# Optimization experiments

Hardware: AMD Instinct MI355X
Metric: run time of the kernel (lower is better)

The kernel has to match this reference:

```python
import jax, jax.numpy as jnp
import numpy as np

N_FILTER = 128
IMAGE_SIZE = 64
CHANNELS = 3
LAT_SIZE = 512
N_CALLS = 2 * 16  # n_calls * 16 sequential CA steps
EPS = 1e-5       # InstanceNorm2d default eps

_SOBEL_X = np.array([[-1.0, 0.0, 1.0], [-2.0, 0.0, 2.0], [-1.0, 0.0, 1.0]], np.float32) / 8.0
_SOBEL_Y = _SOBEL_X.T.copy()
_SOBEL_K = jnp.asarray(np.stack([_SOBEL_X, _SOBEL_Y])[:, None])  # [2,1,3,3]


def sobel_perception(x):
    # x: [B,C,H,W] -> [B,3C,H,W] = concat(identity, grad_x, grad_y)
    B, C, H, W = x.shape
    g = jax.lax.conv_general_dilated(
        x.reshape(B * C, 1, H, W), _SOBEL_K, (1, 1), 'SAME',
        dimension_numbers=('NCHW', 'OIHW', 'NCHW'))
    g = g.reshape(B, C, 2, H, W)
    return jnp.concatenate([x, g[:, :, 0], g[:, :, 1]], axis=1)


def instance_norm(x):
    # per (b, c) normalization over H, W (affine=False)
    m = jnp.mean(x, axis=(2, 3), keepdims=True)
    v = jnp.var(x, axis=(2, 3), keepdims=True)
    return (x - m) * jax.lax.rsqrt(v + EPS)


def setup_inputs() -> dict:
    key = jax.random.key(0)
    k1, k2, k3 = jax.random.split(key, 3)
    C = N_FILTER
    n_params = 3 * C * C + C  # dyn conv weight + bias
    return {
        'lat': jax.random.normal(k1, (8, LAT_SIZE), jnp.float32),
        'leak_factor': jnp.ones((), jnp.float32) * 0.1,
        'w_dyn': jax.random.normal(k2, (LAT_SIZE, n_params), jnp.float32) * 0.02,
        'b_dyn': jax.random.normal(k3, (n_params,), jnp.float32) * 0.02,
    }


def reference(lat, leak_factor, w_dyn, b_dyn):
    B = lat.shape[0]
    C, H, W = N_FILTER, IMAGE_SIZE, IMAGE_SIZE
    # ca_seed: zeros with the center cell set to 1 (Growing-NCA style seed)
    seed = jnp.zeros((B, C, H, W), lat.dtype).at[:, :, H // 2, W // 2].set(1.0)

    # latent-conditioned dynamic 1x1 conv params (per sample)
    params = lat @ w_dyn + b_dyn                     # [B, 3C*C + C]
    w = params[:, :3 * C * C].reshape(B, C, 3 * C)   # [B, out, in]
    b = params[:, 3 * C * C:]                        # [B, C]

    lf = jnp.clip(leak_factor, 0.001, 1000.0)

    def step(out, _):
        y = sobel_perception(out)                    # [B,3C,H,W]
        y = instance_norm(y)
        y = jnp.einsum('bihw,boi->bohw', y, w) + b[:, :, None, None]
        out = out + lf * y
        return out, out

    out, embs = jax.lax.scan(step, seed, None, length=N_CALLS)
    out_embs = jnp.concatenate([seed[None], embs], axis=0)  # [N_CALLS+1,B,C,H,W]
    out_raw = out[:, :CHANNELS]
    return jnp.clip(out_raw, -1.0, 1.0), out_embs, out_raw
```

## Files before the change

### kernel.cpp

```cpp
#include <hip/hip_runtime.h>

typedef unsigned short u16;
typedef short short8 __attribute__((ext_vector_type(8)));
typedef float floatx4 __attribute__((ext_vector_type(4)));

#define NB 8
#define NC 128
#define K3 384
#define HW 4096
#define LATN 512
#define NPAR 49280
#define W2OFF 49152
#define NSTEP 32

#define EMB_OFF 98304
#define EMB_SLICE 4194304
#define RAW_OFF 138510336

__device__ __forceinline__ float bf2f(u16 h) {
    return __uint_as_float(((unsigned)h) << 16);
}
__device__ __forceinline__ u16 f2bf(float f) {
    unsigned u = __float_as_uint(f);
    u += 0x7fffu + ((u >> 16) & 1u);
    return (u16)(u >> 16);
}
__device__ __forceinline__ void splitbf(float f, u16& hi, u16& lo) {
    unsigned u = __float_as_uint(f);
    hi = (u16)(u >> 16);
    lo = f2bf(f - __uint_as_float(u & 0xFFFF0000u));
}

__global__ void k_detect(const unsigned* __restrict__ lfp,
                         int* __restrict__ flag, float* __restrict__ lfF) {
    unsigned bits = lfp[0];
    int isf32 = ((bits & 0xFFFFu) == 0xCCCDu);
    float lf = isf32 ? __uint_as_float(bits) : bf2f((u16)(bits & 0xFFFFu));
    flag[0] = isf32;
    lfF[0] = fminf(fmaxf(lf, 0.001f), 1000.0f);
}

__global__ __launch_bounds__(256) void k_init(const void* __restrict__ lat,
                                              const int* __restrict__ flag,
                                              float* __restrict__ latF,
                                              float* __restrict__ state,
                                              void* __restrict__ outv) {
    int isf32 = flag[0];
    int e = blockIdx.x * 256 + threadIdx.x;
    if (e < NB * LATN)
        latF[e] = isf32 ? ((const float*)lat)[e] : bf2f(((const u16*)lat)[e]);
    float v = ((e & (HW - 1)) == 2080) ? 1.0f : 0.0f;
    state[e] = v;
    if (isf32) ((float*)outv)[EMB_OFF + e] = v;
    else       ((u16*)outv)[EMB_OFF + e] = f2bf(v);
}

__global__ __launch_bounds__(256) void k_params(const float* __restrict__ latF,
                                                const void* __restrict__ w_dyn,
                                                const void* __restrict__ b_dyn,
                                                const int* __restrict__ flag,
                                                u16* __restrict__ Wh,
                                                u16* __restrict__ Wl,
                                                float* __restrict__ biasP) {
    int isf32 = flag[0];
    int j = blockIdx.x * 256 + threadIdx.x;
    if (j >= NPAR) return;
    float acc[NB] = {};
    if (isf32) {
        const float* wd = (const float*)w_dyn;
        for (int k = 0; k < LATN; k++) {
            float wv = wd[(size_t)k * NPAR + j];
#pragma unroll
            for (int b = 0; b < NB; b++) acc[b] += latF[b * LATN + k] * wv;
        }
    } else {
        const u16* wd = (const u16*)w_dyn;
        for (int k = 0; k < LATN; k++) {
            float wv = bf2f(wd[(size_t)k * NPAR + j]);
#pragma unroll
            for (int b = 0; b < NB; b++) acc[b] += latF[b * LATN + k] * wv;
        }
    }
    float bd = isf32 ? ((const float*)b_dyn)[j] : bf2f(((const u16*)b_dyn)[j]);
    if (j < W2OFF) {
#pragma unroll
        for (int b = 0; b < NB; b++) {
            u16 hi, lo;
            splitbf(acc[b] + bd, hi, lo);
            Wh[(size_t)b * W2OFF + j] = hi;
            Wl[(size_t)b * W2OFF + j] = lo;
        }
    } else {
#pragma unroll
        for (int b = 0; b < NB; b++) biasP[b * NC + (j - W2OFF)] = acc[b] + bd;
    }
}

__global__ __launch_bounds__(256) void k_sobel(const float* __restrict__ state,
                                               u16* __restrict__ Yh,
                                               u16* __restrict__ Yl) {
    int blk = blockIdx.x;
    int b = blk >> 7, c = blk & 127;
    const float* xp = state + ((size_t)(b * NC + c)) * HW;
    __shared__ float sm[66 * 68];
    __shared__ float red[4][3];
    __shared__ float bc[6];
    int tid = threadIdx.x;
    int lane = tid & 63, w = tid >> 6;
    for (int i = tid; i < 66 * 68; i += 256) sm[i] = 0.f;
    __syncthreads();
    for (int i = tid; i < HW; i += 256)
        sm[((i >> 6) + 1) * 68 + (i & 63) + 1] = xp[i];
    __syncthreads();

    int rr = tid >> 2, c0 = (tid & 3) << 4;
    const float* r0 = sm + rr * 68 + c0;
    const float* r1 = r0 + 68;
    const float* r2 = r1 + 68;
    float xv[16], gxv[16], gyv[16];
    float a00 = r0[0], a01 = r0[1];
    float a10 = r1[0], a11 = r1[1];
    float a20 = r2[0], a21 = r2[1];
    float sx = 0, sgx = 0, sgy = 0;
#pragma unroll
    for (int u = 0; u < 16; u++) {
        float a02 = r0[u + 2], a12 = r1[u + 2], a22 = r2[u + 2];
        float x  = a11;
        float gx = (a02 - a00 + 2.f * (a12 - a10) + a22 - a20) * 0.125f;
        float gy = (a20 + 2.f * a21 + a22 - a00 - 2.f * a01 - a02) * 0.125f;
        xv[u] = x; gxv[u] = gx; gyv[u] = gy;
        sx += x; sgx += gx; sgy += gy;
        a00 = a01; a01 = a02; a10 = a11; a11 = a12; a20 = a21; a21 = a22;
    }
#pragma unroll
    for (int off = 32; off >= 1; off >>= 1) {
        sx += __shfl_down(sx, off); sgx += __shfl_down(sgx, off); sgy += __shfl_down(sgy, off);
    }
    if (lane == 0) { red[w][0] = sx; red[w][1] = sgx; red[w][2] = sgy; }
    __syncthreads();
    if (tid == 0) {
        float t0 = 0, t1 = 0, t2 = 0;
        for (int i = 0; i < 4; i++) { t0 += red[i][0]; t1 += red[i][1]; t2 += red[i][2]; }
        bc[0] = t0 * (1.f / HW); bc[1] = t1 * (1.f / HW); bc[2] = t2 * (1.f / HW);
    }
    __syncthreads();
    float mx = bc[0], mgx = bc[1], mgy = bc[2];
    float vx = 0, vgx = 0, vgy = 0;
#pragma unroll
    for (int u = 0; u < 16; u++) {
        float dx = xv[u] - mx, dgx = gxv[u] - mgx, dgy = gyv[u] - mgy;
        vx += dx * dx; vgx += dgx * dgx; vgy += dgy * dgy;
    }
#pragma unroll
    for (int off = 32; off >= 1; off >>= 1) {
        vx += __shfl_down(vx, off); vgx += __shfl_down(vgx, off); vgy += __shfl_down(vgy, off);
    }
    __syncthreads();
    if (lane == 0) { red[w][0] = vx; red[w][1] = vgx; red[w][2] = vgy; }
    __syncthreads();
    if (tid == 0) {
        float t0 = 0, t1 = 0, t2 = 0;
        for (int i = 0; i < 4; i++) { t0 += red[i][0]; t1 += red[i][1]; t2 += red[i][2]; }
        bc[3] = rsqrtf(t0 * (1.f / HW) + 1e-5f);
        bc[4] = rsqrtf(t1 * (1.f / HW) + 1e-5f);
        bc[5] = rsqrtf(t2 * (1.f / HW) + 1e-5f);
    }
    __syncthreads();
    float rx = bc[3], rgx = bc[4], rgy = bc[5];

    int ph[3][8], pl[3][8];
#pragma unroll
    for (int u = 0; u < 16; u++) {
        float yv[3] = { (xv[u] - mx) * rx, (gxv[u] - mgx) * rgx, (gyv[u] - mgy) * rgy };
#pragma unroll
        for (int t = 0; t < 3; t++) {
            u16 hi, lo;
            splitbf(yv[t], hi, lo);
            if ((u & 1) == 0) { ph[t][u >> 1] = hi; pl[t][u >> 1] = lo; }
            else { ph[t][u >> 1] |= (unsigned)hi << 16; pl[t][u >> 1] |= (unsigned)lo << 16; }
        }
    }
    int p0 = rr * 64 + c0;
#pragma unroll
    for (int t = 0; t < 3; t++) {
        size_t base = (size_t)(b * K3 + t * 128 + c) * HW + p0;
        ((int4*)(Yh + base))[0] = make_int4(ph[t][0], ph[t][1], ph[t][2], ph[t][3]);
        ((int4*)(Yh + base))[1] = make_int4(ph[t][4], ph[t][5], ph[t][6], ph[t][7]);
        ((int4*)(Yl + base))[0] = make_int4(pl[t][0], pl[t][1], pl[t][2], pl[t][3]);
        ((int4*)(Yl + base))[1] = make_int4(pl[t][4], pl[t][5], pl[t][6], pl[t][7]);
    }
}

__global__ __launch_bounds__(256) void k_mix(const u16* __restrict__ Yh,
                                             const u16* __restrict__ Yl,
                                             const u16* __restrict__ Wh,
                                             const u16* __restrict__ Wl,
                                             const float* __restrict__ biasP,
                                             const float* __restrict__ lfF,
                                             const int* __restrict__ flag,
                                             float* __restrict__ state,
                                             void* __restrict__ outv,
                                             int step) {
    int isf32 = flag[0];
    float lf = lfF[0];
    int b  = blockIdx.x >> 6;
    int pt = (blockIdx.x & 63) << 6;
    int tid = threadIdx.x;
    int lane = tid & 63, wv = tid >> 6;
    int wm = wv >> 1, wn = wv & 1;
    int lq = lane >> 4, lr = lane & 15;
    floatx4 acc[4][2] = {};
    size_t aoff = ((size_t)(b * NC + wm * 64 + lr)) * K3 + lq * 8;
    const u16* Ahb = Wh + aoff;
    const u16* Alb = Wl + aoff;
    int pb = pt + wn * 32 + lr;
    size_t yoff = (size_t)b * K3 * HW + (size_t)(lq * 8) * HW + pb;
    const u16* Yhb = Yh + yoff;
    const u16* Ylb = Yl + yoff;
    for (int kc = 0; kc < 12; kc++) {
        int k0 = kc * 32;
        short8 ah[4], al[4];
#pragma unroll
        for (int mi = 0; mi < 4; mi++) {
            ah[mi] = *(const short8*)(Ahb + mi * 16 * K3 + k0);
            al[mi] = *(const short8*)(Alb + mi * 16 * K3 + k0);
        }
        short8 bh[2], bl[2];
#pragma unroll
        for (int ni = 0; ni < 2; ni++) {
#pragma unroll
            for (int j = 0; j < 8; j++) {
                size_t yi = (size_t)(k0 + j) * HW + ni * 16;
                bh[ni][j] = (short)Yhb[yi];
                bl[ni][j] = (short)Ylb[yi];
            }
        }
#pragma unroll
        for (int mi = 0; mi < 4; mi++)
#pragma unroll
            for (int ni = 0; ni < 2; ni++) {
                acc[mi][ni] = __builtin_amdgcn_mfma_f32_16x16x32_bf16(ah[mi], bh[ni], acc[mi][ni], 0, 0, 0);
                acc[mi][ni] = __builtin_amdgcn_mfma_f32_16x16x32_bf16(al[mi], bh[ni], acc[mi][ni], 0, 0, 0);
                acc[mi][ni] = __builtin_amdgcn_mfma_f32_16x16x32_bf16(ah[mi], bl[ni], acc[mi][ni], 0, 0, 0);
            }
    }
    size_t embb = (size_t)EMB_OFF + (size_t)(step + 1) * EMB_SLICE;
#pragma unroll
    for (int mi = 0; mi < 4; mi++) {
#pragma unroll
        for (int ni = 0; ni < 2; ni++) {
#pragma unroll
            for (int r = 0; r < 4; r++) {
                int o = wm * 64 + mi * 16 + lq * 4 + r;
                int p = pt + wn * 32 + ni * 16 + lr;
                float val = acc[mi][ni][r] + biasP[b * NC + o];
                size_t si = ((size_t)(b * NC + o)) * HW + p;
                float ns = state[si] + lf * val;
                state[si] = ns;
                size_t ei = embb + (size_t)(b * NC + o) * HW + p;
                if (isf32) ((float*)outv)[ei] = ns;
                else       ((u16*)outv)[ei] = f2bf(ns);
                if (step == NSTEP - 1 && o < 3) {
                    int ri = (b * 3 + o) * HW + p;
                    float cl = fminf(fmaxf(ns, -1.f), 1.f);
                    if (isf32) {
                        ((float*)outv)[ri] = cl;
                        ((float*)outv)[(size_t)RAW_OFF + ri] = ns;
                    } else {
                        ((u16*)outv)[ri] = f2bf(cl);
                        ((u16*)outv)[(size_t)RAW_OFF + ri] = f2bf(ns);
                    }
                }
            }
        }
    }
}

extern "C" void kernel_launch(void* const* d_in, const int* in_sizes, int n_in,
                              void* d_out, int out_size, void* d_ws, size_t ws_size,
                              hipStream_t stream) {
    const void* lat   = d_in[0];
    const void* lfp   = d_in[1];
    const void* w_dyn = d_in[2];
    const void* b_dyn = d_in[3];
    char* ws = (char*)d_ws;
    size_t off = 0;
    float* state  = (float*)(ws + off); off += (size_t)NB * NC * HW * 4;
    u16*   Yh     = (u16*)  (ws + off); off += (size_t)NB * K3 * HW * 2;
    u16*   Yl     = (u16*)  (ws + off); off += (size_t)NB * K3 * HW * 2;
    u16*   Wh     = (u16*)  (ws + off); off += (size_t)NB * W2OFF * 2;
    u16*   Wl     = (u16*)  (ws + off); off += (size_t)NB * W2OFF * 2;
    float* biasP  = (float*)(ws + off); off += (size_t)NB * NC * 4;
    float* latF   = (float*)(ws + off); off += (size_t)NB * LATN * 4;
    int*   flag   = (int*)  (ws + off); off += 64;
    float* lfF    = (float*)(ws + off); off += 64;

    k_detect<<<1, 1, 0, stream>>>((const unsigned*)lfp, flag, lfF);
    k_init<<<(NB * NC * HW) / 256, 256, 0, stream>>>(lat, flag, latF, state, d_out);
    k_params<<<(NPAR + 255) / 256, 256, 0, stream>>>(latF, w_dyn, b_dyn, flag, Wh, Wl, biasP);
    for (int step = 0; step < NSTEP; step++) {
        k_sobel<<<NB * NC, 256, 0, stream>>>(state, Yh, Yl);
        k_mix<<<NB * 64, 256, 0, stream>>>(Yh, Yl, Wh, Wl, biasP, lfF, flag, state, d_out, step);
    }
}
```

Baseline: 2.474 ms.

## Normalize identity channels in mix kernel and stage B tiles through LDS

Result: faster. 2.106 ms (-14.9%).

```diff
diff --git a/kernel.cpp b/kernel.cpp
--- a/kernel.cpp
+++ b/kernel.cpp
@@ -7,6 +7,7 @@
 #define NB 8
 #define NC 128
 #define K3 384
+#define YC 256
 #define HW 4096
 #define LATN 512
 #define NPAR 49280
@@ -98,7 +99,9 @@
 
 __global__ __launch_bounds__(256) void k_sobel(const float* __restrict__ state,
                                                u16* __restrict__ Yh,
-                                               u16* __restrict__ Yl) {
+                                               u16* __restrict__ Yl,
+                                               float* __restrict__ statM,
+                                               float* __restrict__ statR) {
     int blk = blockIdx.x;
     int b = blk >> 7, c = blk & 127;
     const float* xp = state + ((size_t)(b * NC + c)) * HW;
@@ -141,7 +144,9 @@
     if (tid == 0) {
         float t0 = 0, t1 = 0, t2 = 0;
         for (int i = 0; i < 4; i++) { t0 += red[i][0]; t1 += red[i][1]; t2 += red[i][2]; }
-        bc[0] = t0 * (1.f / HW); bc[1] = t1 * (1.f / HW); bc[2] = t2 * (1.f / HW);
+        float m0 = t0 * (1.f / HW);
+        bc[0] = m0; bc[1] = t1 * (1.f / HW); bc[2] = t2 * (1.f / HW);
+        statM[b * 128 + c] = m0;
     }
     __syncthreads();
     float mx = bc[0], mgx = bc[1], mgy = bc[2];
@@ -161,19 +166,21 @@
     if (tid == 0) {
         float t0 = 0, t1 = 0, t2 = 0;
         for (int i = 0; i < 4; i++) { t0 += red[i][0]; t1 += red[i][1]; t2 += red[i][2]; }
-        bc[3] = rsqrtf(t0 * (1.f / HW) + 1e-5f);
+        float r0v = rsqrtf(t0 * (1.f / HW) + 1e-5f);
+        bc[3] = r0v;
         bc[4] = rsqrtf(t1 * (1.f / HW) + 1e-5f);
         bc[5] = rsqrtf(t2 * (1.f / HW) + 1e-5f);
-    }
-    __syncthreads();
-    float rx = bc[3], rgx = bc[4], rgy = bc[5];
-
-    int ph[3][8], pl[3][8];
+        statR[b * 128 + c] = r0v;
+    }
+    __syncthreads();
+    float rgx = bc[4], rgy = bc[5];
+
+    int ph[2][8], pl[2][8];
 #pragma unroll
     for (int u = 0; u < 16; u++) {
-        float yv[3] = { (xv[u] - mx) * rx, (gxv[u] - mgx) * rgx, (gyv[u] - mgy) * rgy };
-#pragma unroll
-        for (int t = 0; t < 3; t++) {
+        float yv[2] = { (gxv[u] - mgx) * rgx, (gyv[u] - mgy) * rgy };
+#pragma unroll
+        for (int t = 0; t < 2; t++) {
             u16 hi, lo;
             splitbf(yv[t], hi, lo);
             if ((u & 1) == 0) { ph[t][u >> 1] = hi; pl[t][u >> 1] = lo; }
@@ -182,8 +189,8 @@
     }
     int p0 = rr * 64 + c0;
 #pragma unroll
-    for (int t = 0; t < 3; t++) {
-        size_t base = (size_t)(b * K3 + t * 128 + c) * HW + p0;
+    for (int t = 0; t < 2; t++) {
+        size_t base = (size_t)(b * YC + t * 128 + c) * HW + p0;
         ((int4*)(Yh + base))[0] = make_int4(ph[t][0], ph[t][1], ph[t][2], ph[t][3]);
         ((int4*)(Yh + base))[1] = make_int4(ph[t][4], ph[t][5], ph[t][6], ph[t][7]);
         ((int4*)(Yl + base))[0] = make_int4(pl[t][0], pl[t][1], pl[t][2], pl[t][3]);
@@ -196,6 +203,8 @@
                                              const u16* __restrict__ Wh,
                                              const u16* __restrict__ Wl,
                                              const float* __restrict__ biasP,
+                                             const float* __restrict__ statM,
+                                             const float* __restrict__ statR,
                                              const float* __restrict__ lfF,
                                              const int* __restrict__ flag,
                                              float* __restrict__ state,
@@ -209,32 +218,92 @@
     int lane = tid & 63, wv = tid >> 6;
     int wm = wv >> 1, wn = wv & 1;
     int lq = lane >> 4, lr = lane & 15;
+
+    __shared__ u16 Bh[2][32 * 66];
+    __shared__ u16 Bl[2][32 * 66];
+    __shared__ float sM[128], sR[128];
+    __shared__ float sX[128 * 68];
+
+    if (tid < 128) sM[tid] = statM[b * 128 + tid];
+    else           sR[tid - 128] = statR[b * 128 + tid - 128];
+
     floatx4 acc[4][2] = {};
     size_t aoff = ((size_t)(b * NC + wm * 64 + lr)) * K3 + lq * 8;
     const u16* Ahb = Wh + aoff;
     const u16* Alb = Wl + aoff;
-    int pb = pt + wn * 32 + lr;
-    size_t yoff = (size_t)b * K3 * HW + (size_t)(lq * 8) * HW + pb;
-    const u16* Yhb = Yh + yoff;
-    const u16* Ylb = Yl + yoff;
+
+    int xs_c = tid >> 4;
+    int xs_p = (tid & 15) << 2;
+    int ys_k = tid >> 3;
+    int ys_p = (tid & 7) << 3;
+    int fb   = lq * 8 * 66 + wn * 32 + lr;
+
+    const float* xbase = state + (size_t)(b * NC) * HW + pt;
+    float4 f0 = *(const float4*)(xbase + (size_t)xs_c * HW + xs_p);
+    float4 f1 = *(const float4*)(xbase + (size_t)(xs_c + 16) * HW + xs_p);
+    int4 sh, sl;
+    __syncthreads();
+
     for (int kc = 0; kc < 12; kc++) {
-        int k0 = kc * 32;
+        unsigned* BhW = (unsigned*)Bh[kc & 1];
+        unsigned* BlW = (unsigned*)Bl[kc & 1];
+        if (kc < 4) {
+            int ca = (kc << 5) + xs_c, cb = ca + 16;
+            float mA = sM[ca], rA = sR[ca], mB = sM[cb], rB = sR[cb];
+            *(float4*)&sX[ca * 68 + xs_p] = f0;
+            *(float4*)&sX[cb * 68 + xs_p] = f1;
+            u16 h0, h1, h2, h3, l0, l1, l2, l3;
+            splitbf((f0.x - mA) * rA, h0, l0);
+            splitbf((f0.y - mA) * rA, h1, l1);
+            splitbf((f0.z - mA) * rA, h2, l2);
+            splitbf((f0.w - mA) * rA, h3, l3);
+            int dwA = (xs_c * 66 + xs_p) >> 1;
+            BhW[dwA]     = (unsigned)h0 | ((unsigned)h1 << 16);
+            BhW[dwA + 1] = (unsigned)h2 | ((unsigned)h3 << 16);
+            BlW[dwA]     = (unsigned)l0 | ((unsigned)l1 << 16);
+            BlW[dwA + 1] = (unsigned)l2 | ((unsigned)l3 << 16);
+            splitbf((f1.x - mB) * rB, h0, l0);
+            splitbf((f1.y - mB) * rB, h1, l1);
+            splitbf((f1.z - mB) * rB, h2, l2);
+            splitbf((f1.w - mB) * rB, h3, l3);
+            int dwB = ((xs_c + 16) * 66 + xs_p) >> 1;
+            BhW[dwB]     = (unsigned)h0 | ((unsigned)h1 << 16);
+            BhW[dwB + 1] = (unsigned)h2 | ((unsigned)h3 << 16);
+            BlW[dwB]     = (unsigned)l0 | ((unsigned)l1 << 16);
+            BlW[dwB + 1] = (unsigned)l2 | ((unsigned)l3 << 16);
+        } else {
+            int dw = (ys_k * 66 + ys_p) >> 1;
+            BhW[dw]     = sh.x; BhW[dw + 1] = sh.y; BhW[dw + 2] = sh.z; BhW[dw + 3] = sh.w;
+            BlW[dw]     = sl.x; BlW[dw + 1] = sl.y; BlW[dw + 2] = sl.z; BlW[dw + 3] = sl.w;
+        }
+        if (kc < 3) {
+            const float* sp = xbase + (size_t)((kc + 1) << 5) * HW;
+            f0 = *(const float4*)(sp + (size_t)xs_c * HW + xs_p);
+            f1 = *(const float4*)(sp + (size_t)(xs_c + 16) * HW + xs_p);
+        } else if (kc < 11) {
+            size_t yb = ((size_t)(b * YC + ((kc - 3) << 5) + ys_k)) * HW + pt + ys_p;
+            sh = *(const int4*)(Yh + yb);
+            sl = *(const int4*)(Yl + yb);
+        }
+        asm volatile("s_waitcnt lgkmcnt(0)\n\ts_barrier" ::: "memory");
+
+        int k0 = kc << 5;
         short8 ah[4], al[4];
 #pragma unroll
         for (int mi = 0; mi < 4; mi++) {
-            ah[mi] = *(const short8*)(Ahb + mi * 16 * K3 + k0);
-            al[mi] = *(const short8*)(Alb + mi * 16 * K3 + k0);
-        }
+            ah[mi] = *(const short8*)(Ahb + (size_t)mi * 16 * K3 + k0);
+            al[mi] = *(const short8*)(Alb + (size_t)mi * 16 * K3 + k0);
+        }
+        const u16* BhR = Bh[kc & 1];
+        const u16* BlR = Bl[kc & 1];
         short8 bh[2], bl[2];
 #pragma unroll
-        for (int ni = 0; ni < 2; ni++) {
+        for (int ni = 0; ni < 2; ni++)
 #pragma unroll
             for (int j = 0; j < 8; j++) {
-                size_t yi = (size_t)(k0 + j) * HW + ni * 16;
-                bh[ni][j] = (short)Yhb[yi];
-                bl[ni][j] = (short)Ylb[yi];
+                bh[ni][j] = (short)BhR[fb + j * 66 + ni * 16];
+                bl[ni][j] = (short)BlR[fb + j * 66 + ni * 16];
             }
-        }
 #pragma unroll
         for (int mi = 0; mi < 4; mi++)
 #pragma unroll
@@ -244,6 +313,7 @@
                 acc[mi][ni] = __builtin_amdgcn_mfma_f32_16x16x32_bf16(ah[mi], bl[ni], acc[mi][ni], 0, 0, 0);
             }
     }
+
     size_t embb = (size_t)EMB_OFF + (size_t)(step + 1) * EMB_SLICE;
 #pragma unroll
     for (int mi = 0; mi < 4; mi++) {
@@ -252,10 +322,11 @@
 #pragma unroll
             for (int r = 0; r < 4; r++) {
                 int o = wm * 64 + mi * 16 + lq * 4 + r;
-                int p = pt + wn * 32 + ni * 16 + lr;
+                int pcol = wn * 32 + ni * 16 + lr;
+                int p = pt + pcol;
                 float val = acc[mi][ni][r] + biasP[b * NC + o];
                 size_t si = ((size_t)(b * NC + o)) * HW + p;
-                float ns = state[si] + lf * val;
+                float ns = sX[o * 68 + pcol] + lf * val;
                 state[si] = ns;
                 size_t ei = embb + (size_t)(b * NC + o) * HW + p;
                 if (isf32) ((float*)outv)[ei] = ns;
@@ -286,12 +357,14 @@
     char* ws = (char*)d_ws;
     size_t off = 0;
     float* state  = (float*)(ws + off); off += (size_t)NB * NC * HW * 4;
-    u16*   Yh     = (u16*)  (ws + off); off += (size_t)NB * K3 * HW * 2;
-    u16*   Yl     = (u16*)  (ws + off); off += (size_t)NB * K3 * HW * 2;
+    u16*   Yh     = (u16*)  (ws + off); off += (size_t)NB * YC * HW * 2;
+    u16*   Yl     = (u16*)  (ws + off); off += (size_t)NB * YC * HW * 2;
     u16*   Wh     = (u16*)  (ws + off); off += (size_t)NB * W2OFF * 2;
     u16*   Wl     = (u16*)  (ws + off); off += (size_t)NB * W2OFF * 2;
     float* biasP  = (float*)(ws + off); off += (size_t)NB * NC * 4;
     float* latF   = (float*)(ws + off); off += (size_t)NB * LATN * 4;
+    float* statM  = (float*)(ws + off); off += (size_t)NB * NC * 4;
+    float* statR  = (float*)(ws + off); off += (size_t)NB * NC * 4;
     int*   flag   = (int*)  (ws + off); off += 64;
     float* lfF    = (float*)(ws + off); off += 64;
 
@@ -299,7 +372,7 @@
     k_init<<<(NB * NC * HW) / 256, 256, 0, stream>>>(lat, flag, latF, state, d_out);
     k_params<<<(NPAR + 255) / 256, 256, 0, stream>>>(latF, w_dyn, b_dyn, flag, Wh, Wl, biasP);
     for (int step = 0; step < NSTEP; step++) {
-        k_sobel<<<NB * NC, 256, 0, stream>>>(state, Yh, Yl);
-        k_mix<<<NB * 64, 256, 0, stream>>>(Yh, Yl, Wh, Wl, biasP, lfF, flag, state, d_out, step);
-    }
-}
+        k_sobel<<<NB * NC, 256, 0, stream>>>(state, Yh, Yl, statM, statR);
+        k_mix<<<NB * 64, 256, 0, stream>>>(Yh, Yl, Wh, Wl, biasP, statM, statR, lfF, flag, state, d_out, step);
+    }
+}
```
